# Kernel tuning notes

Hardware: AMD Instinct MI355X
Metric: run time of the kernel (lower is better)

The kernel has to match this reference:

```python
import jax, jax.numpy as jnp
import numpy as np

CTX = 7  # context -> window width 15


def _conv(x, w, b, pad):
    # x: [N,C,H,W], w: [O,I,kH,kW]
    out = jax.lax.conv_general_dilated(
        x, w, window_strides=(1, 1),
        padding=[(pad, pad), (pad, pad)],
        dimension_numbers=("NCHW", "OIHW", "NCHW"))
    return out + b[None, :, None, None]


def _maxpool21(h):
    return jax.lax.reduce_window(h, -jnp.inf, jax.lax.max,
                                 (1, 1, 2, 1), (1, 1, 2, 1), "VALID")


def setup_inputs() -> dict:
    key = jax.random.key(0)
    ks = jax.random.split(key, 18)
    f32 = jnp.float32

    def w(k, shape):
        fan_in = shape[1] * shape[2] * shape[3]
        return (jax.random.normal(k, shape, f32) / np.sqrt(fan_in)).astype(f32)

    B, T, F = 4, 512, 104
    OUT = 25
    inp = {
        "x": jax.random.normal(ks[0], (B, T, F), f32),
        # block 1: four 3x3 convs, 1->32->32->32->32
        "w1a": w(ks[1], (32, 1, 3, 3)),  "b1a": jnp.zeros((32,), f32),
        "w1b": w(ks[2], (32, 32, 3, 3)), "b1b": jnp.zeros((32,), f32),
        "w1c": w(ks[3], (32, 32, 3, 3)), "b1c": jnp.zeros((32,), f32),
        "w1d": w(ks[4], (32, 32, 3, 3)), "b1d": jnp.zeros((32,), f32),
        # block 2: two 3x3 valid convs, 32->64->64
        "w2a": w(ks[5], (64, 32, 3, 3)), "b2a": jnp.zeros((64,), f32),
        "w2b": w(ks[6], (64, 64, 3, 3)), "b2b": jnp.zeros((64,), f32),
        # block 3: (12,9) valid conv, 64->128
        "w3": w(ks[7], (128, 64, 12, 9)), "b3": jnp.zeros((128,), f32),
        # 1x1 conv head, 128->OUT
        "wl": w(ks[8], (OUT, 128, 1, 1)), "bl": jnp.zeros((OUT,), f32),
    }
    return inp


def reference(x, w1a, b1a, w1b, b1b, w1c, b1c, w1d, b1d,
              w2a, b2a, w2b, b2b, w3, b3, wl, bl):
    B, T, F = x.shape
    W = 2 * CTX + 1
    # sliding-window unfold (vectorized version of the Python double loop)
    xp = jnp.pad(jnp.transpose(x, (0, 2, 1)), ((0, 0), (0, 0), (CTX, CTX)))  # [B,F,T+2c]
    idx = jnp.arange(T)[:, None] + jnp.arange(W)[None, :]                    # [T,15]
    win = xp[:, :, idx]                         # [B,F,T,15]
    win = jnp.transpose(win, (0, 2, 1, 3))      # [B,T,F,15]
    h = win.reshape(B * T, 1, F, W)             # [N,1,104,15]

    relu = jax.nn.relu
    # block 1
    h = relu(_conv(h, w1a, b1a, 1))
    h = relu(_conv(h, w1b, b1b, 1))
    h = relu(_conv(h, w1c, b1c, 1))
    h = relu(_conv(h, w1d, b1d, 1))
    h = _maxpool21(h)                           # [N,32,52,15]
    # block 2
    h = relu(_conv(h, w2a, b2a, 0))
    h = relu(_conv(h, w2b, b2b, 0))
    h = _maxpool21(h)                           # [N,64,24,11]
    # block 3
    h = relu(_conv(h, w3, b3, 0))               # [N,128,13,3]
    # 1x1 head
    h = _conv(h, wl, bl, 0)                     # [N,OUT,13,3]
    # avg pool (13,3)
    h = jax.lax.reduce_window(h, jnp.float32(0), jax.lax.add,
                              (1, 1, 13, 3), (1, 1, 13, 3), "VALID") / 39.0
    out = h.reshape(B, T, -1)                   # [B,T,OUT]
    return out
```

## Files before the change

### kernel.cpp

```cpp
#include <hip/hip_runtime.h>

typedef __attribute__((ext_vector_type(8))) short bf16x8;
typedef __attribute__((ext_vector_type(4))) float f32x4;
typedef __attribute__((ext_vector_type(2))) unsigned int u32x2;
typedef __attribute__((ext_vector_type(4))) unsigned int u32x4;

#define MFMA16(a,b,c) __builtin_amdgcn_mfma_f32_16x16x32_bf16((a),(b),(c),0,0,0)

__device__ __forceinline__ unsigned short f2bf(float f){
  union { float f; unsigned u; } v; v.f = f;
  unsigned u = v.u;
  u += 0x7fffu + ((u >> 16) & 1u);
  return (unsigned short)(u >> 16);
}
__device__ __forceinline__ float bf2f(unsigned short h){
  union { unsigned u; float f; } v; v.u = (unsigned)h << 16;
  return v.f;
}
__device__ __forceinline__ unsigned pack2(float a, float b){
  return (unsigned)f2bf(a) | ((unsigned)f2bf(b) << 16);
}
__device__ __forceinline__ float rb(float a, float b){ float v = a + b; return v > 0.f ? v : 0.f; }
__device__ __forceinline__ bf16x8 ld16u(const unsigned short* p){ return *reinterpret_cast<const bf16x8*>(p); }

__global__ void pack_w(const float* __restrict__ w, unsigned short* __restrict__ dst,
                       int CO, int CI, int KH, int KW){
  int K = CI * KH * KW;
  int total = CO * K;
  for (int e = blockIdx.x * blockDim.x + threadIdx.x; e < total; e += gridDim.x * blockDim.x){
    int co = e / K, k = e - co * K;
    int dhw = k / CI, ci = k - dhw * CI;
    int dh = dhw / KW, dw = dhw - dh * KW;
    dst[((k >> 5) * CO + co) * 32 + (k & 31)] = f2bf(w[((co * CI + ci) * KH + dh) * KW + dw]);
  }
}

__global__ void pack_w1a(const float* __restrict__ w, unsigned short* __restrict__ dst){
  int e = blockIdx.x * 256 + threadIdx.x;
  if (e >= 1024) return;
  int co = e >> 5, k = e & 31;
  unsigned short v = 0;
  if (k < 27){
    int j = k < 18 ? (k < 9 ? k : k - 9) : k - 18;
    float wv = w[co * 9 + j];
    unsigned short hi = f2bf(wv);
    v = (k < 18) ? hi : f2bf(wv - bf2f(hi));
  }
  dst[co * 32 + k] = v;
}

__device__ __forceinline__ bf16x8 t1_ld(const unsigned short* buf, int r, int kq, int c){
  return *reinterpret_cast<const bf16x8*>(buf + ((r*4 + kq)*17 + c)*8);
}
__device__ __forceinline__ void t1_st(unsigned short* buf, int r, int px, int kq,
    const f32x4& a0, const f32x4& a1, const float* b0, const float* b1, bool valid){
  int q0 = kq >> 1, half = kq & 1;
  unsigned short* p = buf + ((r*4 + q0)*17 + px + 1)*8 + half*4;
  u32x2 s0, s1;
  s0.x = 0u; s0.y = 0u; s1.x = 0u; s1.y = 0u;
  if (valid){
    s0.x = pack2(rb(a0[0],b0[0]), rb(a0[1],b0[1]));
    s0.y = pack2(rb(a0[2],b0[2]), rb(a0[3],b0[3]));
    s1.x = pack2(rb(a1[0],b1[0]), rb(a1[1],b1[1]));
    s1.y = pack2(rb(a1[2],b1[2]), rb(a1[3],b1[3]));
  }
  *reinterpret_cast<u32x2*>(p) = s0;
  *reinterpret_cast<u32x2*>(p + 272) = s1;
}
__device__ __forceinline__ void t1_sth(unsigned short* buf, int r, int px, int kq, int ct,
    const f32x4& a, const float* b, bool valid){
  int q0 = kq >> 1, half = kq & 1;
  unsigned short* p = buf + ((r*4 + ct*2 + q0)*17 + px + 1)*8 + half*4;
  u32x2 s0; s0.x = 0u; s0.y = 0u;
  if (valid){
    s0.x = pack2(rb(a[0],b[0]), rb(a[1],b[1]));
    s0.y = pack2(rb(a[2],b[2]), rb(a[3],b[3]));
  }
  *reinterpret_cast<u32x2*>(p) = s0;
}

__device__ __forceinline__ void s1_conv(const unsigned short* src, unsigned short* dst,
    const unsigned short* __restrict__ wp, const float* __restrict__ bias,
    int base, int ROW0, int NROWS, int wid, int r16, int kq, int px){
  int ct = wid & 1, rg = wid >> 1;
  bf16x8 w[9];
#pragma unroll
  for (int kb = 0; kb < 9; ++kb)
    w[kb] = ld16u(wp + (kb*32 + ct*16 + r16)*32 + kq*8);
  float b[4];
#pragma unroll
  for (int r = 0; r < 4; ++r) b[r] = bias[ct*16 + kq*4 + r];
  int qn = NROWS >> 2, rem = NROWS & 3;
  int r0 = ROW0 + rg*qn + (rg < rem ? rg : rem);
  int len = qn + (rg < rem ? 1 : 0);
  bf16x8 f[3][3];
#pragma unroll
  for (int dw = 0; dw < 3; ++dw){
    f[0][dw] = t1_ld(src, r0 - 1, kq, px + dw);
    f[1][dw] = t1_ld(src, r0,     kq, px + dw);
  }
#pragma unroll
  for (int i = 0; i < 8; ++i){
    if (i < len){
      int r = r0 + i;
      const int sA = i % 3, sB = (i+1) % 3, sC = (i+2) % 3;
#pragma unroll
      for (int dw = 0; dw < 3; ++dw) f[sC][dw] = t1_ld(src, r + 1, kq, px + dw);
      f32x4 a = {0,0,0,0};
#pragma unroll
      for (int dw = 0; dw < 3; ++dw) a = MFMA16(w[dw],   f[sA][dw], a);
#pragma unroll
      for (int dw = 0; dw < 3; ++dw) a = MFMA16(w[3+dw], f[sB][dw], a);
#pragma unroll
      for (int dw = 0; dw < 3; ++dw) a = MFMA16(w[6+dw], f[sC][dw], a);
      t1_sth(dst, r, px, kq, ct, a, b, (unsigned)(base + r) < 104u);
    }
  }
}

__global__ __launch_bounds__(512)
__attribute__((amdgpu_waves_per_eu(2, 2)))
void fused_k(
    const float* __restrict__ x,
    const unsigned short* __restrict__ wp1a, const float* __restrict__ b1a,
    const unsigned short* __restrict__ wp1b, const float* __restrict__ b1b,
    const unsigned short* __restrict__ wp1c, const float* __restrict__ b1c,
    const unsigned short* __restrict__ wp1d, const float* __restrict__ b1d,
    const unsigned short* __restrict__ wp2a, const float* __restrict__ b2a,
    const unsigned short* __restrict__ wp2b, const float* __restrict__ b2b,
    unsigned short* __restrict__ P2g)
{
  __shared__ __align__(16) char smem[133120];
  unsigned short* s_p1 = (unsigned short*)smem;
  unsigned short* bufA = (unsigned short*)(smem + 49920);
  unsigned short* bufB = (unsigned short*)(smem + 86912);
  float*          xsf  = (float*)(smem + 123904);
  unsigned short* h2a  = (unsigned short*)(smem + 49920);

  const int tid = threadIdx.x;
  const int lane = tid & 63, wid = tid >> 6;
  const int r16 = lane & 15, kq = lane >> 4;
  const int s = blockIdx.x;
  const int bb = s >> 9, tc = s & 511;

  for (int e = tid; e < 544; e += 512){
    int bsel = e & 1, idx = e >> 1;
    int col = idx & 1, rowq = idx >> 1;
    unsigned short* bp = bsel ? bufB : bufA;
    u32x4 z = {0u,0u,0u,0u};
    *reinterpret_cast<u32x4*>(bp + (rowq*17 + col*16)*8) = z;
  }

  const int px15 = r16 < 15 ? r16 : 14;

  bf16x8 wa0 = ld16u(wp1a + r16*32 + kq*8);
  bf16x8 wa1 = ld16u(wp1a + (16 + r16)*32 + kq*8);
  float ba0[4], ba1[4];
#pragma unroll
  for (int r = 0; r < 4; ++r){ ba0[r] = b1a[kq*4 + r]; ba1[r] = b1a[16 + kq*4 + r]; }

  for (int j = 0; j < 4; ++j){
    int base = 26*j - 4;
    for (int e = tid; e < 578; e += 512){
      int ri = e % 34, c = e / 34;
      int h = base + ri, ttx = tc - 8 + c;
      float v = 0.f;
      if ((unsigned)(c - 1) < 15u && (unsigned)h < 104u && (unsigned)ttx < 512u)
        v = x[((size_t)bb*512 + ttx)*104 + h];
      xsf[c*37 + ri] = v;
    }
    __syncthreads();
    {
      int r0 = 1 + wid*4;
      float v[3][3];
#pragma unroll
      for (int dw = 0; dw < 3; ++dw){
        v[0][dw] = xsf[(px15+dw)*37 + r0 - 1];
        v[1][dw] = xsf[(px15+dw)*37 + r0];
      }
#pragma unroll
      for (int i = 0; i < 4; ++i){
        int r = r0 + i;
        const int sA = i % 3, sB = (i+1) % 3, sC = (i+2) % 3;
#pragma unroll
        for (int dw = 0; dw < 3; ++dw) v[sC][dw] = xsf[(px15+dw)*37 + r + 1];
        float q[9] = { v[sA][0], v[sA][1], v[sA][2],
                       v[sB][0], v[sB][1], v[sB][2],
                       v[sC][0], v[sC][1], v[sC][2] };
        unsigned short h[9], l[9];
#pragma unroll
        for (int t = 0; t < 9; ++t){
          h[t] = f2bf(q[t]);
          l[t] = f2bf(q[t] - bf2f(h[t]));
        }
        u32x4 tw = {0u,0u,0u,0u};
        if (kq == 0){
          tw.x = (unsigned)h[0] | ((unsigned)h[1] << 16);
          tw.y = (unsigned)h[2] | ((unsigned)h[3] << 16);
          tw.z = (unsigned)h[4] | ((unsigned)h[5] << 16);
          tw.w = (unsigned)h[6] | ((unsigned)h[7] << 16);
        } else if (kq == 1){
          tw.x = (unsigned)h[8] | ((unsigned)l[0] << 16);
          tw.y = (unsigned)l[1] | ((unsigned)l[2] << 16);
          tw.z = (unsigned)l[3] | ((unsigned)l[4] << 16);
          tw.w = (unsigned)l[5] | ((unsigned)l[6] << 16);
        } else if (kq == 2){
          tw.x = (unsigned)l[7] | ((unsigned)l[8] << 16);
          tw.y = (unsigned)h[0] | ((unsigned)h[1] << 16);
          tw.z = (unsigned)h[2] | ((unsigned)h[3] << 16);
          tw.w = (unsigned)h[4] | ((unsigned)h[5] << 16);
        } else {
          tw.x = (unsigned)h[6] | ((unsigned)h[7] << 16);
          tw.y = (unsigned)h[8];
        }
        bf16x8 bf = *reinterpret_cast<bf16x8*>(&tw);
        f32x4 z = {0,0,0,0};
        f32x4 a0 = MFMA16(wa0, bf, z);
        f32x4 a1 = MFMA16(wa1, bf, z);
        t1_st(bufA, r, px15, kq, a0, a1, ba0, ba1, (unsigned)(base + r) < 104u);
      }
    }
    __syncthreads();
    s1_conv(bufA, bufB, wp1b, b1b, base, 2, 30, wid, r16, kq, px15);
    __syncthreads();
    s1_conv(bufB, bufA, wp1c, b1c, base, 3, 28, wid, r16, kq, px15);
    __syncthreads();
    s1_conv(bufA, bufB, wp1d, b1d, base, 4, 26, wid, r16, kq, px15);
    __syncthreads();
    for (int e = tid; e < 780; e += 512){
      int cg = e & 3, w = (e >> 2) % 15, pr = e / 60;
      const unsigned short* pA = bufB + (((4 + 2*pr)*4 + cg)*17 + w + 1)*8;
      bf16x8 va = *reinterpret_cast<const bf16x8*>(pA);
      bf16x8 vb = *reinterpret_cast<const bf16x8*>(pA + 544);
      bf16x8 rv;
#pragma unroll
      for (int q = 0; q < 8; ++q){
        unsigned short ua = (unsigned short)va[q], ub = (unsigned short)vb[q];
        rv[q] = (short)(ua > ub ? ua : ub);
      }
      *reinterpret_cast<bf16x8*>(s_p1 + (((13*j + pr)*4 + cg)*15 + w)*8) = rv;
    }
    __syncthreads();
  }

  {
    int ct = wid & 3, rh = wid >> 2;
    bf16x8 w2[9];
#pragma unroll
    for (int kb = 0; kb < 9; ++kb)
      w2[kb] = ld16u(wp2a + (kb*64 + ct*16 + r16)*32 + kq*8);
    float bs[4];
#pragma unroll
    for (int r = 0; r < 4; ++r) bs[r] = b2a[ct*16 + kq*4 + r];
    int px = r16 < 13 ? r16 : 12;
    int r0 = rh * 25;
    bf16x8 f[3][3];
#pragma unroll
    for (int dw = 0; dw < 3; ++dw){
      f[0][dw] = *reinterpret_cast<const bf16x8*>(s_p1 + ((r0*4 + kq)*15 + px + dw)*8);
      f[1][dw] = *reinterpret_cast<const bf16x8*>(s_p1 + (((r0+1)*4 + kq)*15 + px + dw)*8);
    }
    int q0 = kq >> 1, half = kq & 1;
#pragma unroll
    for (int i = 0; i < 25; ++i){
      int r = r0 + i;
      const int sA = i % 3, sB = (i+1) % 3, sC = (i+2) % 3;
#pragma unroll
      for (int dw = 0; dw < 3; ++dw)
        f[sC][dw] = *reinterpret_cast<const bf16x8*>(s_p1 + (((r+2)*4 + kq)*15 + px + dw)*8);
      f32x4 a = {0,0,0,0};
#pragma unroll
      for (int dw = 0; dw < 3; ++dw) a = MFMA16(w2[dw],   f[sA][dw], a);
#pragma unroll
      for (int dw = 0; dw < 3; ++dw) a = MFMA16(w2[3+dw], f[sB][dw], a);
#pragma unroll
      for (int dw = 0; dw < 3; ++dw) a = MFMA16(w2[6+dw], f[sC][dw], a);
      u32x2 sv;
      sv.x = pack2(rb(a[0],bs[0]), rb(a[1],bs[1]));
      sv.y = pack2(rb(a[2],bs[2]), rb(a[3],bs[3]));
      *reinterpret_cast<u32x2*>(h2a + ((r*8 + ct*2 + q0)*13 + px)*8 + half*4) = sv;
    }
  }
  __syncthreads();

  {
    int ct = wid & 3, rg = wid >> 2;
    bf16x8 wt[18];
#pragma unroll
    for (int kb = 0; kb < 18; ++kb)
      wt[kb] = ld16u(wp2b + (kb*64 + ct*16 + r16)*32 + kq*8);
    float bt[4];
#pragma unroll
    for (int r = 0; r < 4; ++r) bt[r] = b2b[ct*16 + kq*4 + r];
    int px = r16 < 11 ? r16 : 10;
    int r0 = rg * 24;
    float pv[4];
#pragma unroll
    for (int r4 = 0; r4 < 4; ++r4) pv[r4] = 0.f;
#pragma unroll 2
    for (int i = 0; i < 24; ++i){
      int r = r0 + i;
      f32x4 a0 = {0,0,0,0};
#pragma unroll
      for (int dh = 0; dh < 3; ++dh)
#pragma unroll
        for (int dw = 0; dw < 3; ++dw)
#pragma unroll
          for (int hf = 0; hf < 2; ++hf){
            bf16x8 bf = *reinterpret_cast<const bf16x8*>(h2a + (((r+dh)*8 + hf*4 + kq)*13 + px + dw)*8);
            a0 = MFMA16(wt[(dh*3+dw)*2 + hf], bf, a0);
          }
      if ((i & 1) == 0){
#pragma unroll
        for (int r4 = 0; r4 < 4; ++r4) pv[r4] = rb(a0[r4], bt[r4]);
      } else {
        if (r16 < 11){
          int pp = (r >> 1)*11 + px;
          unsigned short* dp = P2g + (size_t)s*16896 + pp*64 + ct*16 + kq*4;
          u32x2 qv;
          float c0, c1;
          c0 = rb(a0[0], bt[0]); c1 = rb(a0[1], bt[1]);
          qv.x = pack2(pv[0] > c0 ? pv[0] : c0, pv[1] > c1 ? pv[1] : c1);
          c0 = rb(a0[2], bt[2]); c1 = rb(a0[3], bt[3]);
          qv.y = pack2(pv[2] > c0 ? pv[2] : c0, pv[3] > c1 ? pv[3] : c1);
          *reinterpret_cast<u32x2*>(dp) = qv;
        }
      }
    }
  }
}

__global__ __launch_bounds__(512)
__attribute__((amdgpu_waves_per_eu(2, 2)))
void conv3_k(const unsigned short* __restrict__ p2,
      const unsigned short* __restrict__ wp3, const float* __restrict__ b3,
      const float* __restrict__ wl, const float* __restrict__ bl,
      float* __restrict__ out)
{
  __shared__ __align__(16) char smem[137216];
  char* lds = smem;
  float* sbuf = (float*)(smem + 135168);

  const int tid = threadIdx.x;
  const int lane = tid & 63, wid = tid >> 6;
  const int r16 = lane & 15, kq = lane >> 4;
  const int blk = blockIdx.x;

  const unsigned short* src = p2 + (size_t)blk * 4 * 16896;
  for (int c = tid; c < 8448; c += 512){
    int e = c * 8;
    int sl = e / 16896; int er = e - sl * 16896;
    int pix = er >> 6; int cc = (er >> 3) & 7;
    int dstb = sl * 33792 + pix * 128 + ((cc ^ (pix & 7)) << 4);
    *reinterpret_cast<bf16x8*>(lds + dstb) = ld16u(src + e);
  }
  __syncthreads();

  const int tg = wid & 1, sg = (wid >> 1) & 1, par = wid >> 2;
  int ipb[3]; int vm[3];
#pragma unroll
  for (int m = 0; m < 3; ++m){
    int p = m*16 + r16;
    vm[m] = (p < 39);
    int pc = p < 39 ? p : 38;
    int h = pc / 3, w = pc - h*3;
    ipb[m] = h*11 + w;
  }
  f32x4 acc[3][2][4];
#pragma unroll
  for (int m = 0; m < 3; ++m)
#pragma unroll
    for (int ss2 = 0; ss2 < 2; ++ss2)
#pragma unroll
      for (int t4 = 0; t4 < 4; ++t4) acc[m][ss2][t4] = (f32x4){0,0,0,0};

  const unsigned short* wb = wp3 + (size_t)par*4096 + tg*2048 + r16*32 + kq*8;
  bf16x8 wc[4];
#pragma unroll
  for (int t4 = 0; t4 < 4; ++t4) wc[t4] = ld16u(wb + t4*512);
  const int cc0 = par*4 + kq;
  int dh = 0, dw = 0;
  for (int k = 0; k < 108; ++k){
    bf16x8 wn[4];
    if (k < 107){
      const unsigned short* wb2 = wb + (size_t)(k+1)*8192;
#pragma unroll
      for (int t4 = 0; t4 < 4; ++t4) wn[t4] = ld16u(wb2 + t4*512);
    } else {
#pragma unroll
      for (int t4 = 0; t4 < 4; ++t4) wn[t4] = wc[t4];
    }
    int d = dh*11 + dw;
#pragma unroll
    for (int m = 0; m < 3; ++m){
      int ip = ipb[m] + d;
      int bo = ip*128 + ((cc0 ^ (ip & 7)) << 4);
#pragma unroll
      for (int ss2 = 0; ss2 < 2; ++ss2){
        bf16x8 bf = *reinterpret_cast<const bf16x8*>(lds + (sg*2 + ss2)*33792 + bo);
#pragma unroll
        for (int t4 = 0; t4 < 4; ++t4) acc[m][ss2][t4] = MFMA16(wc[t4], bf, acc[m][ss2][t4]);
      }
    }
#pragma unroll
    for (int t4 = 0; t4 < 4; ++t4) wc[t4] = wn[t4];
    if (++dw == 9){ dw = 0; ++dh; }
  }
  __syncthreads();

  f32x4* red = (f32x4*)lds;
  if (par == 1){
#pragma unroll
    for (int m = 0; m < 3; ++m)
#pragma unroll
      for (int ss2 = 0; ss2 < 2; ++ss2)
#pragma unroll
        for (int t4 = 0; t4 < 4; ++t4)
          red[(((tg*2 + sg)*6 + m*2 + ss2)*4 + t4)*64 + lane] = acc[m][ss2][t4];
  }
  __syncthreads();
  if (par == 0){
    float sv[2][4][4];
#pragma unroll
    for (int m = 0; m < 3; ++m)
#pragma unroll
      for (int ss2 = 0; ss2 < 2; ++ss2)
#pragma unroll
        for (int t4 = 0; t4 < 4; ++t4){
          f32x4 o = red[(((tg*2 + sg)*6 + m*2 + ss2)*4 + t4)*64 + lane];
#pragma unroll
          for (int r = 0; r < 4; ++r){
            float v = acc[m][ss2][t4][r] + o[r] + b3[(tg*4 + t4)*16 + kq*4 + r];
            v = v > 0.f ? v : 0.f;
            v = vm[m] ? v : 0.f;
            if (m == 0) sv[ss2][t4][r] = v; else sv[ss2][t4][r] += v;
          }
        }
#pragma unroll
    for (int off = 1; off < 16; off <<= 1)
#pragma unroll
      for (int ss2 = 0; ss2 < 2; ++ss2)
#pragma unroll
        for (int t4 = 0; t4 < 4; ++t4)
#pragma unroll
          for (int r = 0; r < 4; ++r) sv[ss2][t4][r] += __shfl_xor(sv[ss2][t4][r], off, 16);
    if (r16 == 0){
#pragma unroll
      for (int ss2 = 0; ss2 < 2; ++ss2)
#pragma unroll
        for (int t4 = 0; t4 < 4; ++t4)
#pragma unroll
          for (int r = 0; r < 4; ++r)
            sbuf[(sg*2 + ss2)*128 + (tg*4 + t4)*16 + kq*4 + r] = sv[ss2][t4][r];
    }
  }
  __syncthreads();
  if (tid < 100){
    int ss = tid / 25, o = tid - ss*25;
    float a = 0.f;
    for (int c = 0; c < 128; ++c) a += wl[o*128 + c] * sbuf[ss*128 + c];
    out[(size_t)(blk*4 + ss)*25 + o] = a * (1.f/39.f) + bl[o];
  }
}

extern "C" void kernel_launch(void* const* d_in, const int* in_sizes, int n_in,
                              void* d_out, int out_size, void* d_ws, size_t ws_size,
                              hipStream_t stream){
  const float* x   = (const float*)d_in[0];
  const float* w1a = (const float*)d_in[1];  const float* b1a = (const float*)d_in[2];
  const float* w1b = (const float*)d_in[3];  const float* b1b = (const float*)d_in[4];
  const float* w1c = (const float*)d_in[5];  const float* b1c = (const float*)d_in[6];
  const float* w1d = (const float*)d_in[7];  const float* b1d = (const float*)d_in[8];
  const float* w2a = (const float*)d_in[9];  const float* b2a = (const float*)d_in[10];
  const float* w2b = (const float*)d_in[11]; const float* b2b = (const float*)d_in[12];
  const float* w3  = (const float*)d_in[13]; const float* b3  = (const float*)d_in[14];
  const float* wl  = (const float*)d_in[15]; const float* bl  = (const float*)d_in[16];
  float* out = (float*)d_out;

  unsigned short* ws0  = (unsigned short*)d_ws;
  unsigned short* wp1a = ws0;
  unsigned short* wp1b = wp1a + 1024;
  unsigned short* wp1c = wp1b + 9216;
  unsigned short* wp1d = wp1c + 9216;
  unsigned short* wp2a = wp1d + 9216;
  unsigned short* wp2b = wp2a + 18432;
  unsigned short* wp3  = wp2b + 36864;
  unsigned short* P2   = wp3 + 884736;

  pack_w1a<<<4, 256, 0, stream>>>(w1a, wp1a);
  pack_w<<<36,   256, 0, stream>>>(w1b, wp1b, 32, 32, 3, 3);
  pack_w<<<36,   256, 0, stream>>>(w1c, wp1c, 32, 32, 3, 3);
  pack_w<<<36,   256, 0, stream>>>(w1d, wp1d, 32, 32, 3, 3);
  pack_w<<<72,   256, 0, stream>>>(w2a, wp2a, 64, 32, 3, 3);
  pack_w<<<144,  256, 0, stream>>>(w2b, wp2b, 64, 64, 3, 3);
  pack_w<<<3456, 256, 0, stream>>>(w3,  wp3, 128, 64, 12, 9);

  fused_k<<<2048, 512, 0, stream>>>(x, wp1a, b1a, wp1b, b1b, wp1c, b1c, wp1d, b1d,
                                    wp2a, b2a, wp2b, b2b, P2);
  conv3_k<<<512, 512, 0, stream>>>(P2, wp3, b3, wl, bl, out);
}
```

Baseline: 643.5 us.

## Spill pooled block-1 output to global and slice block-2 to halve LDS

The pooled block-1 activations now go to a per-block global scratch buffer instead of LDS. Block 2 runs in two row slices so its intermediate fits in a smaller LDS region, cutting shared memory from about 130KB to about 75KB and raising the waves-per-EU hint to 4. This aims to fit two workgroups per CU for better latency hiding. The cost is extra global/L2 traffic for the block-1 output, a threadfence, more barriers, overlapping halo recompute in conv2a, and possibly several launches if workspace is small.

```diff
diff --git a/kernel.cpp b/kernel.cpp
--- a/kernel.cpp
+++ b/kernel.cpp
@@ -119,7 +119,7 @@
 }
 
 __global__ __launch_bounds__(512)
-__attribute__((amdgpu_waves_per_eu(2, 2)))
+__attribute__((amdgpu_waves_per_eu(4)))
 void fused_k(
     const float* __restrict__ x,
     const unsigned short* __restrict__ wp1a, const float* __restrict__ b1a,
@@ -128,20 +128,20 @@
     const unsigned short* __restrict__ wp1d, const float* __restrict__ b1d,
     const unsigned short* __restrict__ wp2a, const float* __restrict__ b2a,
     const unsigned short* __restrict__ wp2b, const float* __restrict__ b2b,
-    unsigned short* __restrict__ P2g)
+    unsigned short* __restrict__ P1g, unsigned short* __restrict__ P2g, int s0)
 {
-  __shared__ __align__(16) char smem[133120];
-  unsigned short* s_p1 = (unsigned short*)smem;
-  unsigned short* bufA = (unsigned short*)(smem + 49920);
-  unsigned short* bufB = (unsigned short*)(smem + 86912);
-  float*          xsf  = (float*)(smem + 123904);
-  unsigned short* h2a  = (unsigned short*)(smem + 49920);
+  __shared__ __align__(16) char smem[76544];
+  unsigned short* bufA = (unsigned short*)smem;
+  unsigned short* bufB = (unsigned short*)(smem + 36992);
+  float*          xsf  = (float*)(smem + 73984);
+  unsigned short* h2a  = (unsigned short*)smem;
 
   const int tid = threadIdx.x;
   const int lane = tid & 63, wid = tid >> 6;
   const int r16 = lane & 15, kq = lane >> 4;
-  const int s = blockIdx.x;
+  const int s = blockIdx.x + s0;
   const int bb = s >> 9, tc = s & 511;
+  unsigned short* p1s = P1g + (size_t)blockIdx.x * 24960;
 
   for (int e = tid; e < 544; e += 512){
     int bsel = e & 1, idx = e >> 1;
@@ -228,8 +228,8 @@
     s1_conv(bufA, bufB, wp1d, b1d, base, 4, 26, wid, r16, kq, px15);
     __syncthreads();
     for (int e = tid; e < 780; e += 512){
-      int cg = e & 3, w = (e >> 2) % 15, pr = e / 60;
-      const unsigned short* pA = bufB + (((4 + 2*pr)*4 + cg)*17 + w + 1)*8;
+      int w = e % 15; int cgr = (e / 15) & 3; int pr = e / 60;
+      const unsigned short* pA = bufB + (((4 + 2*pr)*4 + cgr)*17 + w + 1)*8;
       bf16x8 va = *reinterpret_cast<const bf16x8*>(pA);
       bf16x8 vb = *reinterpret_cast<const bf16x8*>(pA + 544);
       bf16x8 rv;
@@ -238,94 +238,94 @@
         unsigned short ua = (unsigned short)va[q], ub = (unsigned short)vb[q];
         rv[q] = (short)(ua > ub ? ua : ub);
       }
-      *reinterpret_cast<bf16x8*>(s_p1 + (((13*j + pr)*4 + cg)*15 + w)*8) = rv;
+      *reinterpret_cast<bf16x8*>(p1s + (((13*j + pr)*4 + cgr)*15 + w)*8) = rv;
     }
     __syncthreads();
   }
 
+  __threadfence();
+  __syncthreads();
+
   {
-    int ct = wid & 3, rh = wid >> 2;
-    bf16x8 w2[9];
-#pragma unroll
-    for (int kb = 0; kb < 9; ++kb)
-      w2[kb] = ld16u(wp2a + (kb*64 + ct*16 + r16)*32 + kq*8);
-    float bs[4];
-#pragma unroll
-    for (int r = 0; r < 4; ++r) bs[r] = b2a[ct*16 + kq*4 + r];
-    int px = r16 < 13 ? r16 : 12;
-    int r0 = rh * 25;
-    bf16x8 f[3][3];
-#pragma unroll
-    for (int dw = 0; dw < 3; ++dw){
-      f[0][dw] = *reinterpret_cast<const bf16x8*>(s_p1 + ((r0*4 + kq)*15 + px + dw)*8);
-      f[1][dw] = *reinterpret_cast<const bf16x8*>(s_p1 + (((r0+1)*4 + kq)*15 + px + dw)*8);
-    }
-    int q0 = kq >> 1, half = kq & 1;
-#pragma unroll
-    for (int i = 0; i < 25; ++i){
-      int r = r0 + i;
-      const int sA = i % 3, sB = (i+1) % 3, sC = (i+2) % 3;
-#pragma unroll
-      for (int dw = 0; dw < 3; ++dw)
-        f[sC][dw] = *reinterpret_cast<const bf16x8*>(s_p1 + (((r+2)*4 + kq)*15 + px + dw)*8);
-      f32x4 a = {0,0,0,0};
-#pragma unroll
-      for (int dw = 0; dw < 3; ++dw) a = MFMA16(w2[dw],   f[sA][dw], a);
-#pragma unroll
-      for (int dw = 0; dw < 3; ++dw) a = MFMA16(w2[3+dw], f[sB][dw], a);
-#pragma unroll
-      for (int dw = 0; dw < 3; ++dw) a = MFMA16(w2[6+dw], f[sC][dw], a);
-      u32x2 sv;
-      sv.x = pack2(rb(a[0],bs[0]), rb(a[1],bs[1]));
-      sv.y = pack2(rb(a[2],bs[2]), rb(a[3],bs[3]));
-      *reinterpret_cast<u32x2*>(h2a + ((r*8 + ct*2 + q0)*13 + px)*8 + half*4) = sv;
-    }
-  }
-  __syncthreads();
-
-  {
-    int ct = wid & 3, rg = wid >> 2;
-    bf16x8 wt[18];
-#pragma unroll
-    for (int kb = 0; kb < 18; ++kb)
-      wt[kb] = ld16u(wp2b + (kb*64 + ct*16 + r16)*32 + kq*8);
-    float bt[4];
-#pragma unroll
-    for (int r = 0; r < 4; ++r) bt[r] = b2b[ct*16 + kq*4 + r];
-    int px = r16 < 11 ? r16 : 10;
-    int r0 = rg * 24;
-    float pv[4];
-#pragma unroll
-    for (int r4 = 0; r4 < 4; ++r4) pv[r4] = 0.f;
-#pragma unroll 2
-    for (int i = 0; i < 24; ++i){
-      int r = r0 + i;
-      f32x4 a0 = {0,0,0,0};
-#pragma unroll
-      for (int dh = 0; dh < 3; ++dh)
-#pragma unroll
-        for (int dw = 0; dw < 3; ++dw)
-#pragma unroll
-          for (int hf = 0; hf < 2; ++hf){
-            bf16x8 bf = *reinterpret_cast<const bf16x8*>(h2a + (((r+dh)*8 + hf*4 + kq)*13 + px + dw)*8);
-            a0 = MFMA16(wt[(dh*3+dw)*2 + hf], bf, a0);
-          }
-      if ((i & 1) == 0){
-#pragma unroll
-        for (int r4 = 0; r4 < 4; ++r4) pv[r4] = rb(a0[r4], bt[r4]);
-      } else {
-        if (r16 < 11){
-          int pp = (r >> 1)*11 + px;
-          unsigned short* dp = P2g + (size_t)s*16896 + pp*64 + ct*16 + kq*4;
-          u32x2 qv;
-          float c0, c1;
-          c0 = rb(a0[0], bt[0]); c1 = rb(a0[1], bt[1]);
-          qv.x = pack2(pv[0] > c0 ? pv[0] : c0, pv[1] > c1 ? pv[1] : c1);
-          c0 = rb(a0[2], bt[2]); c1 = rb(a0[3], bt[3]);
-          qv.y = pack2(pv[2] > c0 ? pv[2] : c0, pv[3] > c1 ? pv[3] : c1);
-          *reinterpret_cast<u32x2*>(dp) = qv;
+    const int ct = wid & 3, hi = wid >> 2;
+    const int q0 = kq >> 1, half = kq & 1;
+    const int pxa = r16 < 13 ? r16 : 12;
+    const int pxb = r16 < 11 ? r16 : 10;
+    float bs[4], bt[4];
+#pragma unroll
+    for (int r = 0; r < 4; ++r){ bs[r] = b2a[ct*16 + kq*4 + r]; bt[r] = b2b[ct*16 + kq*4 + r]; }
+
+#pragma unroll 1
+    for (int sl = 0; sl < 2; ++sl){
+      const int hb    = sl ? 26 : 0;
+      const int acnt  = sl ? 12 : 14;
+      const int pA0   = sl ? 13 : 0;
+      const int pSplit= sl ? 19 : 7;
+      const int pEnd  = sl ? 24 : 13;
+
+      {
+        bf16x8 w2[9];
+#pragma unroll
+        for (int kb = 0; kb < 9; ++kb)
+          w2[kb] = ld16u(wp2a + (kb*64 + ct*16 + r16)*32 + kq*8);
+        int rbase = hb + hi * acnt;
+        for (int i = 0; i < acnt; ++i){
+          int r = rbase + i, hr = r - hb;
+          f32x4 a = {0,0,0,0};
+#pragma unroll
+          for (int dh = 0; dh < 3; ++dh)
+#pragma unroll
+            for (int dw = 0; dw < 3; ++dw){
+              bf16x8 bf = *reinterpret_cast<const bf16x8*>(p1s + (((r+dh)*4 + kq)*15 + pxa + dw)*8);
+              a = MFMA16(w2[dh*3+dw], bf, a);
+            }
+          u32x2 sv;
+          sv.x = pack2(rb(a[0],bs[0]), rb(a[1],bs[1]));
+          sv.y = pack2(rb(a[2],bs[2]), rb(a[3],bs[3]));
+          *reinterpret_cast<u32x2*>(h2a + ((hr*8 + ct*2 + q0)*14 + pxa)*8 + half*4) = sv;
         }
       }
+      __syncthreads();
+
+      {
+        bf16x8 wt[18];
+#pragma unroll
+        for (int kb = 0; kb < 18; ++kb)
+          wt[kb] = ld16u(wp2b + (kb*64 + ct*16 + r16)*32 + kq*8);
+        int p0 = hi == 0 ? pA0 : pSplit;
+        int p1 = hi == 0 ? pSplit : pEnd;
+        for (int p = p0; p < p1; ++p){
+          float pv[4];
+#pragma unroll
+          for (int sub = 0; sub < 2; ++sub){
+            int hr = 2*p + sub - hb;
+            f32x4 a0 = {0,0,0,0};
+#pragma unroll
+            for (int dh = 0; dh < 3; ++dh)
+#pragma unroll
+              for (int dw = 0; dw < 3; ++dw)
+#pragma unroll
+                for (int hf = 0; hf < 2; ++hf){
+                  bf16x8 bf = *reinterpret_cast<const bf16x8*>(h2a + (((hr+dh)*8 + hf*4 + kq)*14 + pxb + dw)*8);
+                  a0 = MFMA16(wt[(dh*3+dw)*2 + hf], bf, a0);
+                }
+            if (sub == 0){
+#pragma unroll
+              for (int r4 = 0; r4 < 4; ++r4) pv[r4] = rb(a0[r4], bt[r4]);
+            } else if (r16 < 11){
+              unsigned short* dp = P2g + (size_t)s*16896 + (p*11 + pxb)*64 + ct*16 + kq*4;
+              u32x2 qv;
+              float c0, c1;
+              c0 = rb(a0[0], bt[0]); c1 = rb(a0[1], bt[1]);
+              qv.x = pack2(pv[0] > c0 ? pv[0] : c0, pv[1] > c1 ? pv[1] : c1);
+              c0 = rb(a0[2], bt[2]); c1 = rb(a0[3], bt[3]);
+              qv.y = pack2(pv[2] > c0 ? pv[2] : c0, pv[3] > c1 ? pv[3] : c1);
+              *reinterpret_cast<u32x2*>(dp) = qv;
+            }
+          }
+        }
+      }
+      __syncthreads();
     }
   }
 }
@@ -486,6 +486,11 @@
   unsigned short* wp2b = wp2a + 18432;
   unsigned short* wp3  = wp2b + 36864;
   unsigned short* P2   = wp3 + 884736;
+  unsigned short* P1   = P2 + (size_t)2048 * 16896;
+
+  size_t fixed_shorts = (size_t)(P1 - ws0);
+  int CH = 2048;
+  while (CH > 64 && (fixed_shorts + (size_t)CH * 24960) * 2 > ws_size) CH >>= 1;
 
   pack_w1a<<<4, 256, 0, stream>>>(w1a, wp1a);
   pack_w<<<36,   256, 0, stream>>>(w1b, wp1b, 32, 32, 3, 3);
@@ -495,7 +500,8 @@
   pack_w<<<144,  256, 0, stream>>>(w2b, wp2b, 64, 64, 3, 3);
   pack_w<<<3456, 256, 0, stream>>>(w3,  wp3, 128, 64, 12, 9);
 
-  fused_k<<<2048, 512, 0, stream>>>(x, wp1a, b1a, wp1b, b1b, wp1c, b1c, wp1d, b1d,
-                                    wp2a, b2a, wp2b, b2b, P2);
+  for (int s0 = 0; s0 < 2048; s0 += CH)
+    fused_k<<<CH, 512, 0, stream>>>(x, wp1a, b1a, wp1b, b1b, wp1c, b1c, wp1d, b1d,
+                                    wp2a, b2a, wp2b, b2b, P1, P2, s0);
   conv3_k<<<512, 512, 0, stream>>>(P2, wp3, b3, wl, bl, out);
 }
```

New measurement: 1.592 ms. 147% more time.
